# Performance work log

Measured on AMD Instinct MI355X. Metric: run time of the kernel, lower is better.

## Reference

```python
import jax, jax.numpy as jnp
import numpy as np

HIDDEN = 1024
NUM_HEADS = 16
HEAD_DIM = HIDDEN // NUM_HEADS
B, S = 4, 4096


def setup_inputs() -> dict:
    key = jax.random.key(0)
    ks = jax.random.split(key, 7)
    scale = 1.0 / np.sqrt(HIDDEN)
    return {
        "hidden_states": jax.random.normal(ks[0], (B, S, HIDDEN), dtype=jnp.float32),
        "Wq": jax.random.normal(ks[1], (HIDDEN, HIDDEN), dtype=jnp.float32) * scale,
        "bq": jax.random.normal(ks[2], (HIDDEN,), dtype=jnp.float32) * 0.01,
        "Wk": jax.random.normal(ks[3], (HIDDEN, HIDDEN), dtype=jnp.float32) * scale,
        "bk": jax.random.normal(ks[4], (HIDDEN,), dtype=jnp.float32) * 0.01,
        "Wv": jax.random.normal(ks[5], (HIDDEN, HIDDEN), dtype=jnp.float32) * scale,
        "bv": jax.random.normal(ks[6], (HIDDEN,), dtype=jnp.float32) * 0.01,
    }


def _split_heads(x):
    # [B, S, H*D] -> [B, H, S, D]
    b, s, _ = x.shape
    return x.reshape(b, s, NUM_HEADS, HEAD_DIM).transpose(0, 2, 1, 3)


def reference(hidden_states, Wq, bq, Wk, bk, Wv, bv):
    # Fused-style QKV: single stacked GEMM, then split + reshape to heads.
    Wqkv = jnp.concatenate([Wq, Wk, Wv], axis=1)          # [H, 3H]
    bqkv = jnp.concatenate([bq, bk, bv], axis=0)           # [3H]
    qkv = jnp.einsum("bsh,hf->bsf", hidden_states, Wqkv) + bqkv  # [B, S, 3H]
    q, k, v = jnp.split(qkv, 3, axis=-1)
    return (_split_heads(q), _split_heads(k), _split_heads(v))
```

## Files before the change

kernel.cpp:

```cpp
#include <hip/hip_runtime.h>
#include <hip/hip_bf16.h>


#define M_TOT 16384
#define N_TOT 3072
#define K_TOT 1024

typedef __bf16 bf16x8 __attribute__((ext_vector_type(8)));
typedef float f32x16 __attribute__((ext_vector_type(16)));

#define AS1(p) ((const __attribute__((address_space(1))) void*)(p))
#define AS3(p) ((__attribute__((address_space(3))) void*)(p))

__device__ __forceinline__ unsigned short f2bf(float f) {
    unsigned int u = __builtin_bit_cast(unsigned int, f);
    u += 0x7fffu + ((u >> 16) & 1u);
    return (unsigned short)(u >> 16);
}

__global__ void convert_hidden(const float* __restrict__ x,
                               unsigned short* __restrict__ y, int n4) {
    int i = blockIdx.x * blockDim.x + threadIdx.x;
    int stride = gridDim.x * blockDim.x;
    for (; i < n4; i += stride) {
        float4 v = ((const float4*)x)[i];
        ushort4 o;
        o.x = f2bf(v.x); o.y = f2bf(v.y); o.z = f2bf(v.z); o.w = f2bf(v.w);
        ((ushort4*)y)[i] = o;
    }
}

__global__ void convert_weights(const float* __restrict__ Wq,
                                const float* __restrict__ Wk,
                                const float* __restrict__ Wv,
                                unsigned short* __restrict__ Bt) {
    __shared__ unsigned short tile[64][65];
    const float* W = (blockIdx.z == 0) ? Wq : (blockIdx.z == 1) ? Wk : Wv;
    int k0 = blockIdx.y * 64;
    int f0 = blockIdx.x * 64;
    int tx = threadIdx.x & 63;
    int ty = threadIdx.x >> 6;
#pragma unroll
    for (int r = 0; r < 16; ++r) {
        int k = ty + r * 4;
        tile[k][tx] = f2bf(W[(size_t)(k0 + k) * 1024 + f0 + tx]);
    }
    __syncthreads();
#pragma unroll
    for (int r = 0; r < 16; ++r) {
        int fr = ty + r * 4;
        Bt[(size_t)(blockIdx.z * 1024 + f0 + fr) * 1024 + k0 + tx] = tile[tx][fr];
    }
}

__launch_bounds__(256, 2)
__global__ void qkv_gemm(const unsigned short* __restrict__ A,
                         const unsigned short* __restrict__ Bt,
                         const float* __restrict__ bq,
                         const float* __restrict__ bk,
                         const float* __restrict__ bv,
                         float* __restrict__ out) {
    __shared__ __align__(16) unsigned short As[128 * 32];
    __shared__ __align__(16) unsigned short Bs[128 * 32];

    const int tid  = threadIdx.x;
    const int wave = tid >> 6;
    const int lane = tid & 63;
    const int r5   = lane & 31;
    const int half = lane >> 5;

    const int bm = blockIdx.x;
    const int bn = blockIdx.y;

    const int wr = wave >> 1;
    const int wc = wave & 1;

    f32x16 acc[2][2] = {};

    const int c0 = wave * 64 + lane;
    const int rowA0 = c0 >> 2;
    const int k8A0  = ((c0 & 3) ^ ((rowA0 >> 1) & 3)) * 8;
    const int c1 = 256 + c0;
    const int rowA1 = c1 >> 2;
    const int k8A1  = ((c1 & 3) ^ ((rowA1 >> 1) & 3)) * 8;

    const unsigned short* gA0 = A  + (size_t)(bm * 128 + rowA0) * 1024 + k8A0;
    const unsigned short* gA1 = A  + (size_t)(bm * 128 + rowA1) * 1024 + k8A1;
    const unsigned short* gB0 = Bt + (size_t)(bn * 128 + rowA0) * 1024 + k8A0;
    const unsigned short* gB1 = Bt + (size_t)(bn * 128 + rowA1) * 1024 + k8A1;

    unsigned short* ldsA0 = As + (size_t)(wave)*512;
    unsigned short* ldsA1 = As + (size_t)(4 + wave) * 512;
    unsigned short* ldsB0 = Bs + (size_t)(wave)*512;
    unsigned short* ldsB1 = Bs + (size_t)(4 + wave) * 512;

    const int swsel = (r5 >> 1) & 3;

    for (int k0 = 0; k0 < K_TOT; k0 += 32) {
        __builtin_amdgcn_global_load_lds(AS1(gA0 + k0), AS3(ldsA0), 16, 0, 0);
        __builtin_amdgcn_global_load_lds(AS1(gA1 + k0), AS3(ldsA1), 16, 0, 0);
        __builtin_amdgcn_global_load_lds(AS1(gB0 + k0), AS3(ldsB0), 16, 0, 0);
        __builtin_amdgcn_global_load_lds(AS1(gB1 + k0), AS3(ldsB1), 16, 0, 0);
        __syncthreads();

        bf16x8 av[2][2], bvv[2][2];
#pragma unroll
        for (int ib = 0; ib < 2; ++ib) {
            int arow = wr * 64 + ib * 32 + r5;
#pragma unroll
            for (int ks = 0; ks < 2; ++ks) {
                int p = (ks * 2 + half) ^ swsel;
                av[ib][ks] = *(const bf16x8*)&As[arow * 32 + p * 8];
            }
        }
#pragma unroll
        for (int jb = 0; jb < 2; ++jb) {
            int brow = wc * 64 + jb * 32 + r5;
#pragma unroll
            for (int ks = 0; ks < 2; ++ks) {
                int p = (ks * 2 + half) ^ swsel;
                bvv[jb][ks] = *(const bf16x8*)&Bs[brow * 32 + p * 8];
            }
        }
#pragma unroll
        for (int ks = 0; ks < 2; ++ks)
#pragma unroll
            for (int ib = 0; ib < 2; ++ib)
#pragma unroll
                for (int jb = 0; jb < 2; ++jb)
                    acc[ib][jb] = __builtin_amdgcn_mfma_f32_32x32x16_bf16(
                        av[ib][ks], bvv[jb][ks], acc[ib][jb], 0, 0, 0);
        __syncthreads();
    }

    const int section = (bn * 128) >> 10;
    const int nloc0   = (bn * 128 - section * 1024) + wc * 64;
    const float* bias = (section == 0) ? bq : (section == 1) ? bk : bv;
    float* outsec = out + (size_t)section * (4u * 16u * 4096u * 64u);

#pragma unroll
    for (int jb = 0; jb < 2; ++jb) {
        int f = nloc0 + jb * 32 + r5;
        float bval = bias[f];
        int h = f >> 6, d = f & 63;
        size_t hb = (size_t)h * (4096u * 64u);
#pragma unroll
        for (int ib = 0; ib < 2; ++ib) {
            int mbase = bm * 128 + wr * 64 + ib * 32 + 4 * half;
#pragma unroll
            for (int reg = 0; reg < 16; ++reg) {
                int m = mbase + (reg & 3) + 8 * (reg >> 2);
                int b = m >> 12, s = m & 4095;
                outsec[(size_t)b * (16u * 4096u * 64u) + hb + (size_t)s * 64u + d] =
                    acc[ib][jb][reg] + bval;
            }
        }
    }
}

extern "C" void kernel_launch(void* const* d_in, const int* in_sizes, int n_in,
                              void* d_out, int out_size, void* d_ws, size_t ws_size,
                              hipStream_t stream) {
    const float* hs = (const float*)d_in[0];
    const float* Wq = (const float*)d_in[1];
    const float* bq = (const float*)d_in[2];
    const float* Wk = (const float*)d_in[3];
    const float* bk = (const float*)d_in[4];
    const float* Wv = (const float*)d_in[5];
    const float* bv = (const float*)d_in[6];
    float* out = (float*)d_out;

    unsigned short* Abf  = (unsigned short*)d_ws;
    unsigned short* Btbf = Abf + (size_t)M_TOT * K_TOT;

    convert_hidden<<<2048, 256, 0, stream>>>(hs, Abf, (M_TOT * K_TOT) / 4);
    convert_weights<<<dim3(16, 16, 3), 256, 0, stream>>>(Wq, Wk, Wv, Btbf);
    qkv_gemm<<<dim3(M_TOT / 128, N_TOT / 128), 256, 0, stream>>>(Abf, Btbf, bq, bk, bv, out);
}
```

Before: 373.8 us.

## Enlarge GEMM tiles to 256x256 with double-buffered LDS prefetch pipeline

The QKV GEMM now uses 256x256 output tiles with 8 waves and a K-step of 64. Global-to-LDS loads for the next K tile are double-buffered and interleaved with MFMA work, using explicit waitcnt and barriers. A remapped 1D grid groups workgroups so neighbouring blocks share operand tiles in cache, and setprio raises priority around the MFMA bursts. This targets load latency and per-tile overhead, at the cost of 128KB of LDS per block and lower occupancy.

Result: slower. 389.9 us (+4.3%).

```diff
diff --git a/kernel.cpp b/kernel.cpp
--- a/kernel.cpp
+++ b/kernel.cpp
@@ -53,15 +53,15 @@
     }
 }
 
-__launch_bounds__(256, 2)
+__launch_bounds__(512, 2)
 __global__ void qkv_gemm(const unsigned short* __restrict__ A,
                          const unsigned short* __restrict__ Bt,
                          const float* __restrict__ bq,
                          const float* __restrict__ bk,
                          const float* __restrict__ bv,
                          float* __restrict__ out) {
-    __shared__ __align__(16) unsigned short As[128 * 32];
-    __shared__ __align__(16) unsigned short Bs[128 * 32];
+    __shared__ __align__(16) unsigned short As[2][16384];
+    __shared__ __align__(16) unsigned short Bs[2][16384];
 
     const int tid  = threadIdx.x;
     const int wave = tid >> 6;
@@ -69,72 +69,86 @@
     const int r5   = lane & 31;
     const int half = lane >> 5;
 
-    const int bm = blockIdx.x;
-    const int bn = blockIdx.y;
+    const int orig = blockIdx.x;
+    const int wg   = (orig & 7) * 96 + (orig >> 3);
+    const int bm   = wg & 63;
+    const int bn   = wg >> 6;
 
-    const int wr = wave >> 1;
-    const int wc = wave & 1;
+    const int wr = wave >> 2;
+    const int wc = wave & 3;
 
-    f32x16 acc[2][2] = {};
+    f32x16 acc[4][2] = {};
 
-    const int c0 = wave * 64 + lane;
-    const int rowA0 = c0 >> 2;
-    const int k8A0  = ((c0 & 3) ^ ((rowA0 >> 1) & 3)) * 8;
-    const int c1 = 256 + c0;
-    const int rowA1 = c1 >> 2;
-    const int k8A1  = ((c1 & 3) ^ ((rowA1 >> 1) & 3)) * 8;
+    const int trow = tid >> 3;
+    const int tkq8 = ((tid & 7) ^ (trow & 7)) * 8;
+    const unsigned short* gA = A  + (size_t)(bm * 256 + trow) * 1024 + tkq8;
+    const unsigned short* gB = Bt + (size_t)(bn * 256 + trow) * 1024 + tkq8;
 
-    const unsigned short* gA0 = A  + (size_t)(bm * 128 + rowA0) * 1024 + k8A0;
-    const unsigned short* gA1 = A  + (size_t)(bm * 128 + rowA1) * 1024 + k8A1;
-    const unsigned short* gB0 = Bt + (size_t)(bn * 128 + rowA0) * 1024 + k8A0;
-    const unsigned short* gB1 = Bt + (size_t)(bn * 128 + rowA1) * 1024 + k8A1;
+#define STAGE(i, koff, dstA, dstB)                                              \
+    do {                                                                        \
+        __builtin_amdgcn_global_load_lds(                                       \
+            AS1(gA + (size_t)(i)*65536 + (koff)),                               \
+            AS3((dstA) + ((i)*512 + wave * 64) * 8), 16, 0, 0);                 \
+        __builtin_amdgcn_global_load_lds(                                       \
+            AS1(gB + (size_t)(i)*65536 + (koff)),                               \
+            AS3((dstB) + ((i)*512 + wave * 64) * 8), 16, 0, 0);                 \
+    } while (0)
 
-    unsigned short* ldsA0 = As + (size_t)(wave)*512;
-    unsigned short* ldsA1 = As + (size_t)(4 + wave) * 512;
-    unsigned short* ldsB0 = Bs + (size_t)(wave)*512;
-    unsigned short* ldsB1 = Bs + (size_t)(4 + wave) * 512;
+#pragma unroll
+    for (int i = 0; i < 4; ++i) STAGE(i, 0, As[0], Bs[0]);
 
-    const int swsel = (r5 >> 1) & 3;
+#pragma unroll 2
+    for (int t = 0; t < 16; ++t) {
+        const int cur = t & 1;
+        const int nxt = cur ^ 1;
+        const bool pf = (t < 15);
+        const int koff = (t + 1) * 64;
+        const unsigned short* Ab = As[cur];
+        const unsigned short* Bb = Bs[cur];
 
-    for (int k0 = 0; k0 < K_TOT; k0 += 32) {
-        __builtin_amdgcn_global_load_lds(AS1(gA0 + k0), AS3(ldsA0), 16, 0, 0);
-        __builtin_amdgcn_global_load_lds(AS1(gA1 + k0), AS3(ldsA1), 16, 0, 0);
-        __builtin_amdgcn_global_load_lds(AS1(gB0 + k0), AS3(ldsB0), 16, 0, 0);
-        __builtin_amdgcn_global_load_lds(AS1(gB1 + k0), AS3(ldsB1), 16, 0, 0);
-        __syncthreads();
-
-        bf16x8 av[2][2], bvv[2][2];
 #pragma unroll
-        for (int ib = 0; ib < 2; ++ib) {
-            int arow = wr * 64 + ib * 32 + r5;
+        for (int ks = 0; ks < 4; ++ks) {
+            bf16x8 av[4], bvv[2];
+            const int prd = ((ks * 2 + half) ^ (r5 & 7)) * 8;
+            if (ks == 0) {
+                if (pf) STAGE(0, koff, As[nxt], Bs[nxt]);
+                if (pf) asm volatile("s_waitcnt vmcnt(2)" ::: "memory");
+                else    asm volatile("s_waitcnt vmcnt(0)" ::: "memory");
+                __builtin_amdgcn_s_barrier();
+                __builtin_amdgcn_sched_barrier(0);
 #pragma unroll
-            for (int ks = 0; ks < 2; ++ks) {
-                int p = (ks * 2 + half) ^ swsel;
-                av[ib][ks] = *(const bf16x8*)&As[arow * 32 + p * 8];
+                for (int ib = 0; ib < 4; ++ib)
+                    av[ib] = *(const bf16x8*)&Ab[(wr * 128 + ib * 32 + r5) * 64 + prd];
+#pragma unroll
+                for (int jb = 0; jb < 2; ++jb)
+                    bvv[jb] = *(const bf16x8*)&Bb[(wc * 64 + jb * 32 + r5) * 64 + prd];
+            } else {
+#pragma unroll
+                for (int ib = 0; ib < 4; ++ib)
+                    av[ib] = *(const bf16x8*)&Ab[(wr * 128 + ib * 32 + r5) * 64 + prd];
+#pragma unroll
+                for (int jb = 0; jb < 2; ++jb)
+                    bvv[jb] = *(const bf16x8*)&Bb[(wc * 64 + jb * 32 + r5) * 64 + prd];
+                if (pf) STAGE(ks, koff, As[nxt], Bs[nxt]);
+                __builtin_amdgcn_s_barrier();
             }
-        }
+            asm volatile("s_waitcnt lgkmcnt(0)" ::: "memory");
+            __builtin_amdgcn_sched_barrier(0);
+            __builtin_amdgcn_s_setprio(1);
 #pragma unroll
-        for (int jb = 0; jb < 2; ++jb) {
-            int brow = wc * 64 + jb * 32 + r5;
-#pragma unroll
-            for (int ks = 0; ks < 2; ++ks) {
-                int p = (ks * 2 + half) ^ swsel;
-                bvv[jb][ks] = *(const bf16x8*)&Bs[brow * 32 + p * 8];
-            }
-        }
-#pragma unroll
-        for (int ks = 0; ks < 2; ++ks)
-#pragma unroll
-            for (int ib = 0; ib < 2; ++ib)
+            for (int ib = 0; ib < 4; ++ib)
 #pragma unroll
                 for (int jb = 0; jb < 2; ++jb)
                     acc[ib][jb] = __builtin_amdgcn_mfma_f32_32x32x16_bf16(
-                        av[ib][ks], bvv[jb][ks], acc[ib][jb], 0, 0, 0);
-        __syncthreads();
+                        av[ib], bvv[jb], acc[ib][jb], 0, 0, 0);
+            __builtin_amdgcn_s_setprio(0);
+            __builtin_amdgcn_s_barrier();
+        }
     }
+#undef STAGE
 
-    const int section = (bn * 128) >> 10;
-    const int nloc0   = (bn * 128 - section * 1024) + wc * 64;
+    const int section = bn >> 2;
+    const int nloc0   = (bn & 3) * 256 + wc * 64;
     const float* bias = (section == 0) ? bq : (section == 1) ? bk : bv;
     float* outsec = out + (size_t)section * (4u * 16u * 4096u * 64u);
 
@@ -145,8 +159,8 @@
         int h = f >> 6, d = f & 63;
         size_t hb = (size_t)h * (4096u * 64u);
 #pragma unroll
-        for (int ib = 0; ib < 2; ++ib) {
-            int mbase = bm * 128 + wr * 64 + ib * 32 + 4 * half;
+        for (int ib = 0; ib < 4; ++ib) {
+            int mbase = bm * 256 + wr * 128 + ib * 32 + 4 * half;
 #pragma unroll
             for (int reg = 0; reg < 16; ++reg) {
                 int m = mbase + (reg & 3) + 8 * (reg >> 2);
@@ -175,5 +189,5 @@
 
     convert_hidden<<<2048, 256, 0, stream>>>(hs, Abf, (M_TOT * K_TOT) / 4);
     convert_weights<<<dim3(16, 16, 3), 256, 0, stream>>>(Wq, Wk, Wv, Btbf);
-    qkv_gemm<<<dim3(M_TOT / 128, N_TOT / 128), 256, 0, stream>>>(Abf, Btbf, bq, bk, bv, out);
+    qkv_gemm<<<dim3((M_TOT / 256) * (N_TOT / 256)), 512, 0, stream>>>(Abf, Btbf, bq, bk, bv, out);
 }
```
